# Kernel tuning notes

Hardware: AMD Instinct MI355X
Metric: run time of the kernel (lower is better)

## Reference

```python
import jax, jax.numpy as jnp
import numpy as np

B, S1, S2, H, HM = 16, 128, 256, 256, 512  # batch, seq1, seq2, per-token hidden, mlp hidden


def setup_inputs() -> dict:
    k = jax.random.key(0)
    ks = jax.random.split(k, 7)
    query = jax.random.normal(ks[0], (B, S1, H), jnp.float32)
    key = jax.random.normal(ks[1], (B, S2, H), jnp.float32)
    value = jax.random.normal(ks[2], (B, S2, H), jnp.float32)
    q_mask = jax.random.randint(ks[3], (B, S1), 0, 2).astype(jnp.float32)
    k_mask = jax.random.randint(ks[4], (B, S2), 0, 2).astype(jnp.float32)
    s1 = 1.0 / np.sqrt(2 * H)
    W1 = jax.random.uniform(ks[5], (2 * H, HM), jnp.float32, -s1, s1)
    b1 = jnp.zeros((HM,), jnp.float32)
    s2 = 1.0 / np.sqrt(HM)
    W2 = jax.random.uniform(ks[6], (HM, 1), jnp.float32, -s2, s2)
    b2 = jnp.zeros((1,), jnp.float32)
    return {"query": query, "key": key, "value": value, "q_mask": q_mask,
            "k_mask": k_mask, "W1": W1, "b1": b1, "W2": W2, "b2": b2}


def reference(query, key, value, q_mask, k_mask, W1, b1, W2, b2):
    # Factor the first Linear over the concat: cat([q,k]) @ W1 == q @ W1[:H] + k @ W1[H:]
    Hq = query.shape[-1]
    qp = jnp.einsum('bqd,dh->bqh', query, W1[:Hq])      # [B,S1,HM]
    kp = jnp.einsum('bkd,dh->bkh', key, W1[Hq:])        # [B,S2,HM]
    hid = jax.nn.relu(qp[:, :, None, :] + kp[:, None, :, :] + b1)  # [B,S1,S2,HM]
    scores = jnp.einsum('bqkh,h->bqk', hid, W2[:, 0]) + b2[0]       # [B,S1,S2]
    mask = q_mask[:, :, None] * k_mask[:, None, :]                   # [B,S1,S2]
    # masked_fill(-inf).exp() == 0 at masked positions
    A = jnp.where(mask == 0, jnp.zeros((), scores.dtype), jnp.exp(scores))
    A_sum = jnp.clip(jnp.sum(A, axis=-1, keepdims=True), 2e-15, None)
    attn = A / A_sum
    return jnp.einsum('bqk,bkd->bqd', attn, value)  # [B,S1,H]
```

## Files before the change

### kernel.cpp

```cpp
#include <hip/hip_runtime.h>
#include <hip/hip_bf16.h>

#define B_  16
#define S1_ 128
#define S2_ 256
#define H_  256
#define HM_ 512
#define QB  4

typedef _Float16 hf2 __attribute__((ext_vector_type(2)));
typedef _Float16 hf4 __attribute__((ext_vector_type(4)));
typedef _Float16 hf8 __attribute__((ext_vector_type(8)));
typedef float    f32x4 __attribute__((ext_vector_type(4)));

static __device__ inline hf2 u2h(unsigned u) {
    union { unsigned u; hf2 h; } x; x.u = u; return x.h;
}

static __device__ inline float dot2(hf2 a, hf2 b, float c) {
#if __has_builtin(__builtin_amdgcn_fdot2)
    return __builtin_amdgcn_fdot2(a, b, c, false);
#else
    asm("v_dot2_f32_f16 %0, %1, %2, %0" : "+v"(c) : "v"(a), "v"(b));
    return c;
#endif
}

__global__ __launch_bounds__(256) void cvtW_kernel(
    const float* __restrict__ W1, _Float16* __restrict__ Wt)
{
    const int u = blockIdx.x * 256 + threadIdx.x;
    const int n = u >> 9, k = u & 511;
    Wt[u] = (_Float16)W1[(size_t)k * HM_ + n];
}

__global__ __launch_bounds__(256) void proj_mfma_kernel(
    const float* __restrict__ query,
    const float* __restrict__ key,
    const _Float16* __restrict__ Wt,
    const float* __restrict__ b1,
    _Float16* __restrict__ QPh,
    _Float16* __restrict__ KPTh)
{
    __shared__ _Float16 Xs[64][40];
    __shared__ _Float16 Ws[64][40];

    const int t   = threadIdx.x;
    const int bid = blockIdx.x;
    const bool modeK = bid >= 256;
    const int lb    = modeK ? bid - 256 : bid;
    const int mtile = lb >> 3, ntile = lb & 7;
    const int m0 = mtile * 64, n0 = ntile * 64;
    const float* X = modeK ? key : query;
    const int kw = modeK ? 256 : 0;

    const int srow = t >> 2;
    const int schk = t & 3;

    const float*    xsrc = X  + (size_t)(m0 + srow) * H_  + schk * 8;
    const _Float16* wsrc = Wt + (size_t)(n0 + srow) * HM_ + kw + schk * 8;

    float4 xa = *(const float4*)xsrc;
    float4 xb = *(const float4*)(xsrc + 4);
    uint4  wv = *(const uint4*)wsrc;

    f32x4 acc[4] = {};

    const int lane = t & 63, wid = t >> 6;
    const int fr = lane & 15;
    const int fk = (lane >> 4) * 8;

    for (int s = 0; s < 8; ++s) {
        __syncthreads();
        hf8 xh = { (_Float16)xa.x, (_Float16)xa.y, (_Float16)xa.z, (_Float16)xa.w,
                   (_Float16)xb.x, (_Float16)xb.y, (_Float16)xb.z, (_Float16)xb.w };
        *(hf8*)&Xs[srow][schk * 8]  = xh;
        *(uint4*)&Ws[srow][schk * 8] = wv;
        __syncthreads();

        if (s < 7) {
            xa = *(const float4*)(xsrc + (s + 1) * 32);
            xb = *(const float4*)(xsrc + (s + 1) * 32 + 4);
            wv = *(const uint4*)(wsrc + (s + 1) * 32);
        }

        hf8 a = *(const hf8*)&Xs[wid * 16 + fr][fk];
#pragma unroll
        for (int nf = 0; nf < 4; ++nf) {
            hf8 b = *(const hf8*)&Ws[nf * 16 + fr][fk];
            acc[nf] = __builtin_amdgcn_mfma_f32_16x16x32_f16(a, b, acc[nf], 0, 0, 0);
        }
    }

    if (!modeK) {
#pragma unroll
        for (int nf = 0; nf < 4; ++nf) {
            const int n = n0 + nf * 16 + fr;
#pragma unroll
            for (int r = 0; r < 4; ++r) {
                const int m = m0 + wid * 16 + (lane >> 4) * 4 + r;
                QPh[(size_t)m * HM_ + n] = (_Float16)acc[nf][r];
            }
        }
    } else {
#pragma unroll
        for (int nf = 0; nf < 4; ++nf) {
            const int n = n0 + nf * 16 + fr;
            const float bv = b1[n];
#pragma unroll
            for (int r = 0; r < 4; ++r) {
                const int m    = m0 + wid * 16 + (lane >> 4) * 4 + r;
                const int bb   = m >> 8, kloc = m & 255;
                KPTh[(((size_t)bb * 64 + (n >> 3)) * 256 + kloc) * 8 + (n & 7)] =
                    (_Float16)(acc[nf][r] + bv);
            }
        }
    }
}

__global__ __launch_bounds__(512, 4) void attn_kernel(
    const _Float16* __restrict__ QPh,
    const _Float16* __restrict__ KPTh,
    const float* __restrict__ value,
    const float* __restrict__ q_mask,
    const float* __restrict__ k_mask,
    const float* __restrict__ W2,
    const float* __restrict__ b2,
    float* __restrict__ out)
{
    __shared__ __align__(16) _Float16 qp_h[QB][HM_];
    __shared__ __align__(16) _Float16 w2_h[HM_];
    __shared__ __align__(16) float    Ap[2][QB][S2_];
    __shared__ __align__(16) float4   opart[8][QB][64];
    __shared__ float rA_s[QB];
    __shared__ float qm_s[QB];
    __shared__ float km_s[S2_];

    const int t  = threadIdx.x;
    const int k  = t & 255;
    const int hb = t >> 8;

    const int orig = blockIdx.x + (int)gridDim.x * blockIdx.y;
    const int wg   = (orig & 7) * 64 + (orig >> 3);
    const int q0   = (wg & 31) * QB;
    const int b    = wg >> 5;

    {
        if (t < 256) {
            const uint4* src = (const uint4*)(QPh + (size_t)(b * S1_ + q0) * HM_);
            ((uint4*)&qp_h[0][0])[t] = src[t];
            km_s[t] = k_mask[b * S2_ + t];
        } else if (t < 256 + 128) {
            const int i = t - 256;
            float4 wvv = ((const float4*)W2)[i];
            hf4 hv = { (_Float16)wvv.x, (_Float16)wvv.y,
                       (_Float16)wvv.z, (_Float16)wvv.w };
            *(hf4*)&w2_h[i * 4] = hv;
        } else if (t < 256 + 128 + QB) {
            const int i = t - (256 + 128);
            qm_s[i] = q_mask[b * S1_ + q0 + i];
        }
    }
    __syncthreads();

    float accs[QB] = {0.f, 0.f, 0.f, 0.f};
    const uint4* kp8 = (const uint4*)KPTh + ((size_t)b * 64 + hb * 32) * S2_ + k;

    for (int c = 0; c < 32; ++c) {
        uint4 kvu = kp8[(size_t)c * S2_];
        const int hoff = hb * (HM_ / 2) + c * 8;
        uint4 w4u = *(const uint4*)&w2_h[hoff];
        hf2 kv0 = u2h(kvu.x), kv1 = u2h(kvu.y), kv2 = u2h(kvu.z), kv3 = u2h(kvu.w);
        hf2 wv0 = u2h(w4u.x), wv1 = u2h(w4u.y), wv2 = u2h(w4u.z), wv3 = u2h(w4u.w);
        const hf2 zero = (hf2)(_Float16)0;
#pragma unroll
        for (int q = 0; q < QB; ++q) {
            uint4 qvu = *(const uint4*)&qp_h[q][hoff];
            hf2 s;
            s = __builtin_elementwise_max(u2h(qvu.x) + kv0, zero);
            accs[q] = dot2(s, wv0, accs[q]);
            s = __builtin_elementwise_max(u2h(qvu.y) + kv1, zero);
            accs[q] = dot2(s, wv1, accs[q]);
            s = __builtin_elementwise_max(u2h(qvu.z) + kv2, zero);
            accs[q] = dot2(s, wv2, accs[q]);
            s = __builtin_elementwise_max(u2h(qvu.w) + kv3, zero);
            accs[q] = dot2(s, wv3, accs[q]);
        }
    }
#pragma unroll
    for (int q = 0; q < QB; ++q) Ap[hb][q][k] = accs[q];
    __syncthreads();

    {
        const float b2v = b2[0];
#pragma unroll
        for (int i = 0; i < 2; ++i) {
            const int idx = t + i * 512;
            const int q = idx >> 8, kk = idx & 255;
            float sc = Ap[0][q][kk] + Ap[1][q][kk] + b2v;
            Ap[0][q][kk] = (qm_s[q] * km_s[kk] == 0.f) ? 0.f : __expf(sc);
        }
    }
    __syncthreads();

    if (t < QB * 64) {
        const int q = t >> 6, lane = t & 63;
        float p = Ap[0][q][lane] + Ap[0][q][lane + 64] +
                  Ap[0][q][lane + 128] + Ap[0][q][lane + 192];
#pragma unroll
        for (int m = 32; m >= 1; m >>= 1) p += __shfl_xor(p, m, 64);
        if (lane == 0) rA_s[q] = 1.0f / fmaxf(p, 2e-15f);
    }
    __syncthreads();

    {
        const int w = t >> 6, lane = t & 63;
        const float4* vb = (const float4*)(value + (size_t)b * S2_ * H_)
                           + (size_t)(w * 32) * (H_ / 4) + lane;
        float4 o[QB];
#pragma unroll
        for (int q = 0; q < QB; ++q) o[q] = make_float4(0.f, 0.f, 0.f, 0.f);
#pragma unroll 4
        for (int kk = 0; kk < 32; ++kk) {
            float4 v = vb[(size_t)kk * (H_ / 4)];
#pragma unroll
            for (int q = 0; q < QB; ++q) {
                float a = Ap[0][q][w * 32 + kk];
                o[q].x = fmaf(a, v.x, o[q].x); o[q].y = fmaf(a, v.y, o[q].y);
                o[q].z = fmaf(a, v.z, o[q].z); o[q].w = fmaf(a, v.w, o[q].w);
            }
        }
#pragma unroll
        for (int q = 0; q < QB; ++q) opart[w][q][lane] = o[q];
    }
    __syncthreads();

    if (t < QB * 64) {
        const int q = t >> 6, lane = t & 63;
        float4 s = make_float4(0.f, 0.f, 0.f, 0.f);
#pragma unroll
        for (int w = 0; w < 8; ++w) {
            float4 p = opart[w][q][lane];
            s.x += p.x; s.y += p.y; s.z += p.z; s.w += p.w;
        }
        const float r = rA_s[q];
        s.x *= r; s.y *= r; s.z *= r; s.w *= r;
        *(float4*)(out + (size_t)(b * S1_ + q0 + q) * H_ + lane * 4) = s;
    }
}

extern "C" void kernel_launch(void* const* d_in, const int* in_sizes, int n_in,
                              void* d_out, int out_size, void* d_ws, size_t ws_size,
                              hipStream_t stream) {
    const float* query  = (const float*)d_in[0];
    const float* key    = (const float*)d_in[1];
    const float* value  = (const float*)d_in[2];
    const float* q_mask = (const float*)d_in[3];
    const float* k_mask = (const float*)d_in[4];
    const float* W1     = (const float*)d_in[5];
    const float* b1     = (const float*)d_in[6];
    const float* W2     = (const float*)d_in[7];
    const float* b2     = (const float*)d_in[8];
    float*       out    = (float*)d_out;

    _Float16* QPh  = (_Float16*)d_ws;
    _Float16* KPTh = QPh  + (size_t)B_ * S1_ * HM_;
    _Float16* Wt   = KPTh + (size_t)B_ * S2_ * HM_;

    cvtW_kernel<<<1024, 256, 0, stream>>>(W1, Wt);

    proj_mfma_kernel<<<768, 256, 0, stream>>>(query, key, Wt, b1, QPh, KPTh);

    attn_kernel<<<dim3(S1_ / QB, B_), 512, 0, stream>>>(
        QPh, KPTh, value, q_mask, k_mask, W2, b2, out);
}
```

Measured before the change: 41.94 us.

## Tile W1 transpose through LDS and load full K panel in projection GEMM

The W1 fp16 conversion kernel now transposes 32x32 tiles through padded shared memory with float4 loads and hf4 stores, replacing strided scalar gathers. The projection GEMM loads the whole 64x256 X and W panels into LDS once, with a single barrier, instead of a double-synchronised 32-wide K loop. Each wave now computes a 2x2 grid of 16x16 MFMA tiles, which reuses the A and B fragments it loads. The cost is much more LDS per block, which may lower occupancy, and the global loads no longer overlap with compute.

```diff
diff --git a/kernel.cpp b/kernel.cpp
--- a/kernel.cpp
+++ b/kernel.cpp
@@ -29,9 +29,23 @@
 __global__ __launch_bounds__(256) void cvtW_kernel(
     const float* __restrict__ W1, _Float16* __restrict__ Wt)
 {
-    const int u = blockIdx.x * 256 + threadIdx.x;
-    const int n = u >> 9, k = u & 511;
-    Wt[u] = (_Float16)W1[(size_t)k * HM_ + n];
+    __shared__ float Ls[32][33];
+    const int t  = threadIdx.x;
+    const int kt = blockIdx.x & 15, nt = blockIdx.x >> 4;
+
+    {
+        const int r = t >> 3, c4 = (t & 7) * 4;
+        float4 v = *(const float4*)(W1 + (size_t)(kt * 32 + r) * HM_ + nt * 32 + c4);
+        Ls[r][c4 + 0] = v.x; Ls[r][c4 + 1] = v.y;
+        Ls[r][c4 + 2] = v.z; Ls[r][c4 + 3] = v.w;
+    }
+    __syncthreads();
+    {
+        const int n = t >> 3, k4 = (t & 7) * 4;
+        hf4 h = { (_Float16)Ls[k4 + 0][n], (_Float16)Ls[k4 + 1][n],
+                  (_Float16)Ls[k4 + 2][n], (_Float16)Ls[k4 + 3][n] };
+        *(hf4*)(Wt + (size_t)(nt * 32 + n) * HM_ + kt * 32 + k4) = h;
+    }
 }
 
 __global__ __launch_bounds__(256) void proj_mfma_kernel(
@@ -42,8 +56,8 @@
     _Float16* __restrict__ QPh,
     _Float16* __restrict__ KPTh)
 {
-    __shared__ _Float16 Xs[64][40];
-    __shared__ _Float16 Ws[64][40];
+    __shared__ _Float16 Xh[64][264];
+    __shared__ _Float16 Wh[64][264];
 
     const int t   = threadIdx.x;
     const int bid = blockIdx.x;
@@ -54,65 +68,66 @@
     const float* X = modeK ? key : query;
     const int kw = modeK ? 256 : 0;
 
-    const int srow = t >> 2;
-    const int schk = t & 3;
-
-    const float*    xsrc = X  + (size_t)(m0 + srow) * H_  + schk * 8;
-    const _Float16* wsrc = Wt + (size_t)(n0 + srow) * HM_ + kw + schk * 8;
-
-    float4 xa = *(const float4*)xsrc;
-    float4 xb = *(const float4*)(xsrc + 4);
-    uint4  wv = *(const uint4*)wsrc;
-
-    f32x4 acc[4] = {};
+#pragma unroll 2
+    for (int i = 0; i < 8; ++i) {
+        const int g   = t + i * 256;
+        const int row = g >> 5, c8 = (g & 31) * 8;
+        float4 xa = *(const float4*)(X + (size_t)(m0 + row) * H_ + c8);
+        float4 xb = *(const float4*)(X + (size_t)(m0 + row) * H_ + c8 + 4);
+        hf8 xh = { (_Float16)xa.x, (_Float16)xa.y, (_Float16)xa.z, (_Float16)xa.w,
+                   (_Float16)xb.x, (_Float16)xb.y, (_Float16)xb.z, (_Float16)xb.w };
+        *(hf8*)&Xh[row][c8] = xh;
+        uint4 wv = *(const uint4*)(Wt + (size_t)(n0 + row) * HM_ + kw + c8);
+        *(uint4*)&Wh[row][c8] = wv;
+    }
+    __syncthreads();
 
     const int lane = t & 63, wid = t >> 6;
+    const int wr = (wid >> 1) * 32;
+    const int wc = (wid & 1) * 32;
     const int fr = lane & 15;
     const int fk = (lane >> 4) * 8;
 
+    f32x4 acc[2][2] = {};
+
+#pragma unroll
     for (int s = 0; s < 8; ++s) {
-        __syncthreads();
-        hf8 xh = { (_Float16)xa.x, (_Float16)xa.y, (_Float16)xa.z, (_Float16)xa.w,
-                   (_Float16)xb.x, (_Float16)xb.y, (_Float16)xb.z, (_Float16)xb.w };
-        *(hf8*)&Xs[srow][schk * 8]  = xh;
-        *(uint4*)&Ws[srow][schk * 8] = wv;
-        __syncthreads();
-
-        if (s < 7) {
-            xa = *(const float4*)(xsrc + (s + 1) * 32);
-            xb = *(const float4*)(xsrc + (s + 1) * 32 + 4);
-            wv = *(const uint4*)(wsrc + (s + 1) * 32);
-        }
-
-        hf8 a = *(const hf8*)&Xs[wid * 16 + fr][fk];
-#pragma unroll
-        for (int nf = 0; nf < 4; ++nf) {
-            hf8 b = *(const hf8*)&Ws[nf * 16 + fr][fk];
-            acc[nf] = __builtin_amdgcn_mfma_f32_16x16x32_f16(a, b, acc[nf], 0, 0, 0);
-        }
+        const int kb = s * 32 + fk;
+        hf8 a0 = *(const hf8*)&Xh[wr + fr][kb];
+        hf8 a1 = *(const hf8*)&Xh[wr + 16 + fr][kb];
+        hf8 b0 = *(const hf8*)&Wh[wc + fr][kb];
+        hf8 b1v = *(const hf8*)&Wh[wc + 16 + fr][kb];
+        acc[0][0] = __builtin_amdgcn_mfma_f32_16x16x32_f16(a0, b0,  acc[0][0], 0, 0, 0);
+        acc[0][1] = __builtin_amdgcn_mfma_f32_16x16x32_f16(a0, b1v, acc[0][1], 0, 0, 0);
+        acc[1][0] = __builtin_amdgcn_mfma_f32_16x16x32_f16(a1, b0,  acc[1][0], 0, 0, 0);
+        acc[1][1] = __builtin_amdgcn_mfma_f32_16x16x32_f16(a1, b1v, acc[1][1], 0, 0, 0);
     }
 
     if (!modeK) {
 #pragma unroll
-        for (int nf = 0; nf < 4; ++nf) {
-            const int n = n0 + nf * 16 + fr;
+        for (int i = 0; i < 2; ++i)
+#pragma unroll
+        for (int j = 0; j < 2; ++j) {
+            const int n = n0 + wc + j * 16 + fr;
 #pragma unroll
             for (int r = 0; r < 4; ++r) {
-                const int m = m0 + wid * 16 + (lane >> 4) * 4 + r;
-                QPh[(size_t)m * HM_ + n] = (_Float16)acc[nf][r];
+                const int m = m0 + wr + i * 16 + (lane >> 4) * 4 + r;
+                QPh[(size_t)m * HM_ + n] = (_Float16)acc[i][j][r];
             }
         }
     } else {
 #pragma unroll
-        for (int nf = 0; nf < 4; ++nf) {
-            const int n = n0 + nf * 16 + fr;
+        for (int i = 0; i < 2; ++i)
+#pragma unroll
+        for (int j = 0; j < 2; ++j) {
+            const int n = n0 + wc + j * 16 + fr;
             const float bv = b1[n];
 #pragma unroll
             for (int r = 0; r < 4; ++r) {
-                const int m    = m0 + wid * 16 + (lane >> 4) * 4 + r;
+                const int m    = m0 + wr + i * 16 + (lane >> 4) * 4 + r;
                 const int bb   = m >> 8, kloc = m & 255;
                 KPTh[(((size_t)bb * 64 + (n >> 3)) * 256 + kloc) * 8 + (n & 7)] =
-                    (_Float16)(acc[nf][r] + bv);
+                    (_Float16)(acc[i][j][r] + bv);
             }
         }
     }
@@ -267,7 +282,7 @@
     _Float16* KPTh = QPh  + (size_t)B_ * S1_ * HM_;
     _Float16* Wt   = KPTh + (size_t)B_ * S2_ * HM_;
 
-    cvtW_kernel<<<1024, 256, 0, stream>>>(W1, Wt);
+    cvtW_kernel<<<256, 256, 0, stream>>>(W1, Wt);
 
     proj_mfma_kernel<<<768, 256, 0, stream>>>(query, key, Wt, b1, QPh, KPTh);
 
```

Result: slower. 42.94 us (+2.4%).

## Pre-swizzle W1 into MFMA fragment layout and read B operands directly from global

Applied to the files above, without the earlier changes.

The weight-conversion kernel now writes W1 as fp16 in the exact per-lane MFMA B-fragment order, so the projection kernel can load B operands straight from global memory (L2-resident) with no LDS staging. Each projection block now covers 16 rows and all 512 output columns with 8 waves, staging only the 16-row fp16 input tile in LDS once. This removes the per-k-step double barriers and LDS traffic for weights, and cuts the grid from 768 to 384 blocks. The cost is more global/L2 weight reads per block and less input reuse across columns, plus a conversion kernel that makes strided 8-element reads.

```diff
diff --git a/kernel.cpp b/kernel.cpp
--- a/kernel.cpp
+++ b/kernel.cpp
@@ -26,90 +26,86 @@
 #endif
 }
 
-__global__ __launch_bounds__(256) void cvtW_kernel(
-    const float* __restrict__ W1, _Float16* __restrict__ Wt)
+__global__ __launch_bounds__(256) void cvtWB_kernel(
+    const float* __restrict__ W1, _Float16* __restrict__ WB)
 {
-    const int u = blockIdx.x * 256 + threadIdx.x;
-    const int n = u >> 9, k = u & 511;
-    Wt[u] = (_Float16)W1[(size_t)k * HM_ + n];
-}
-
-__global__ __launch_bounds__(256) void proj_mfma_kernel(
+    const int idx  = blockIdx.x * 256 + threadIdx.x;
+    const int lane = idx & 63;
+    const int nblk = (idx >> 6) & 31;
+    const int kblk = idx >> 11;
+    const int n    = nblk * 16 + (lane & 15);
+    const int k0   = kblk * 32 + (lane >> 4) * 8;
+    hf8 v;
+#pragma unroll
+    for (int j = 0; j < 8; ++j)
+        v[j] = (_Float16)W1[(size_t)(k0 + j) * HM_ + n];
+    *(hf8*)(WB + (size_t)idx * 8) = v;
+}
+
+__global__ __launch_bounds__(512, 4) void proj_mfma_kernel(
     const float* __restrict__ query,
     const float* __restrict__ key,
-    const _Float16* __restrict__ Wt,
+    const _Float16* __restrict__ WB,
     const float* __restrict__ b1,
     _Float16* __restrict__ QPh,
     _Float16* __restrict__ KPTh)
 {
-    __shared__ _Float16 Xs[64][40];
-    __shared__ _Float16 Ws[64][40];
+    __shared__ _Float16 Xh[16][264];
 
     const int t   = threadIdx.x;
     const int bid = blockIdx.x;
-    const bool modeK = bid >= 256;
-    const int lb    = modeK ? bid - 256 : bid;
-    const int mtile = lb >> 3, ntile = lb & 7;
-    const int m0 = mtile * 64, n0 = ntile * 64;
+    const bool modeK = bid >= 128;
+    const int m0  = (modeK ? bid - 128 : bid) * 16;
     const float* X = modeK ? key : query;
-    const int kw = modeK ? 256 : 0;
-
-    const int srow = t >> 2;
-    const int schk = t & 3;
-
-    const float*    xsrc = X  + (size_t)(m0 + srow) * H_  + schk * 8;
-    const _Float16* wsrc = Wt + (size_t)(n0 + srow) * HM_ + kw + schk * 8;
-
-    float4 xa = *(const float4*)xsrc;
-    float4 xb = *(const float4*)(xsrc + 4);
-    uint4  wv = *(const uint4*)wsrc;
-
-    f32x4 acc[4] = {};
-
-    const int lane = t & 63, wid = t >> 6;
+    const int kb  = modeK ? 8 : 0;
+
+    {
+        const int row = t >> 5, c8 = (t & 31) * 8;
+        const float* xs = X + (size_t)(m0 + row) * H_ + c8;
+        float4 xa = *(const float4*)xs;
+        float4 xb = *(const float4*)(xs + 4);
+        hf8 xh = { (_Float16)xa.x, (_Float16)xa.y, (_Float16)xa.z, (_Float16)xa.w,
+                   (_Float16)xb.x, (_Float16)xb.y, (_Float16)xb.z, (_Float16)xb.w };
+        *(hf8*)&Xh[row][c8] = xh;
+    }
+    __syncthreads();
+
+    const int lane = t & 63, w = t >> 6;
     const int fr = lane & 15;
     const int fk = (lane >> 4) * 8;
 
+    f32x4 acc[4] = {};
+
+#pragma unroll
     for (int s = 0; s < 8; ++s) {
-        __syncthreads();
-        hf8 xh = { (_Float16)xa.x, (_Float16)xa.y, (_Float16)xa.z, (_Float16)xa.w,
-                   (_Float16)xb.x, (_Float16)xb.y, (_Float16)xb.z, (_Float16)xb.w };
-        *(hf8*)&Xs[srow][schk * 8]  = xh;
-        *(uint4*)&Ws[srow][schk * 8] = wv;
-        __syncthreads();
-
-        if (s < 7) {
-            xa = *(const float4*)(xsrc + (s + 1) * 32);
-            xb = *(const float4*)(xsrc + (s + 1) * 32 + 4);
-            wv = *(const uint4*)(wsrc + (s + 1) * 32);
-        }
-
-        hf8 a = *(const hf8*)&Xs[wid * 16 + fr][fk];
+        hf8 a = *(const hf8*)&Xh[fr][s * 32 + fk];
+        const _Float16* bp =
+            WB + ((((size_t)(kb + s) * 32 + w * 4) * 64) + lane) * 8;
 #pragma unroll
         for (int nf = 0; nf < 4; ++nf) {
-            hf8 b = *(const hf8*)&Ws[nf * 16 + fr][fk];
-            acc[nf] = __builtin_amdgcn_mfma_f32_16x16x32_f16(a, b, acc[nf], 0, 0, 0);
+            hf8 bv = *(const hf8*)(bp + (size_t)nf * 64 * 8);
+            acc[nf] = __builtin_amdgcn_mfma_f32_16x16x32_f16(a, bv, acc[nf], 0, 0, 0);
         }
     }
 
     if (!modeK) {
 #pragma unroll
         for (int nf = 0; nf < 4; ++nf) {
-            const int n = n0 + nf * 16 + fr;
+            const int n = w * 64 + nf * 16 + fr;
 #pragma unroll
             for (int r = 0; r < 4; ++r) {
-                const int m = m0 + wid * 16 + (lane >> 4) * 4 + r;
+                const int m = m0 + (lane >> 4) * 4 + r;
                 QPh[(size_t)m * HM_ + n] = (_Float16)acc[nf][r];
             }
         }
     } else {
 #pragma unroll
         for (int nf = 0; nf < 4; ++nf) {
-            const int n = n0 + nf * 16 + fr;
+            const int n = w * 64 + nf * 16 + fr;
             const float bv = b1[n];
 #pragma unroll
             for (int r = 0; r < 4; ++r) {
-                const int m    = m0 + wid * 16 + (lane >> 4) * 4 + r;
+                const int m    = m0 + (lane >> 4) * 4 + r;
                 const int bb   = m >> 8, kloc = m & 255;
                 KPTh[(((size_t)bb * 64 + (n >> 3)) * 256 + kloc) * 8 + (n & 7)] =
                     (_Float16)(acc[nf][r] + bv);
@@ -265,11 +261,11 @@
 
     _Float16* QPh  = (_Float16*)d_ws;
     _Float16* KPTh = QPh  + (size_t)B_ * S1_ * HM_;
-    _Float16* Wt   = KPTh + (size_t)B_ * S2_ * HM_;
-
-    cvtW_kernel<<<1024, 256, 0, stream>>>(W1, Wt);
-
-    proj_mfma_kernel<<<768, 256, 0, stream>>>(query, key, Wt, b1, QPh, KPTh);
+    _Float16* WB   = KPTh + (size_t)B_ * S2_ * HM_;
+
+    cvtWB_kernel<<<128, 256, 0, stream>>>(W1, WB);
+
+    proj_mfma_kernel<<<384, 512, 0, stream>>>(query, key, WB, b1, QPh, KPTh);
 
     attn_kernel<<<dim3(S1_ / QB, B_), 512, 0, stream>>>(
         QPh, KPTh, value, q_mask, k_mask, W2, b2, out);
```

Result: faster. 40.94 us (-2.4%).
